# Performance work log

Measured on AMD Instinct MI355X. Metric: run time of the kernel, lower is better.

The kernel has to match this reference:

```python
import jax, jax.numpy as jnp
import numpy as np

D_MODEL = 1024
N_HEADS = 16
N_KV = 4
HEAD_DIM = D_MODEL // N_HEADS  # 64
EPS = 1e-5
THETA = 10000.0


def _rope_tables(S):
    half = HEAD_DIM // 2
    inv_freq = 1.0 / (THETA ** (jnp.arange(half, dtype=jnp.float32) / half))
    t = jnp.arange(S, dtype=jnp.float32)
    f = t[:, None] * inv_freq[None, :]  # [S, half]
    return jnp.cos(f), jnp.sin(f)


def _apply_rope(x, cos, sin):
    # x: [B, H, S, D]
    half = x.shape[-1] // 2
    x1, x2 = x[..., :half], x[..., half:]
    c = cos[None, None, :, :]
    s = sin[None, None, :, :]
    return jnp.concatenate([x1 * c - x2 * s, x1 * s + x2 * c], axis=-1)


def _rmsnorm(x, scale):
    rms = jnp.sqrt(jnp.mean(x * x, axis=-1, keepdims=True) + EPS)
    return x / rms * scale


def setup_inputs() -> dict:
    key = jax.random.key(0)
    ks = jax.random.split(key, 4)
    B, S = 2, 2048
    x = jax.random.normal(ks[0], (B, S, D_MODEL), dtype=jnp.float32)
    Wq = jax.random.normal(ks[1], (D_MODEL, D_MODEL), dtype=jnp.float32) * 0.02
    Wkv = jax.random.normal(ks[2], (D_MODEL, 2 * N_KV * HEAD_DIM), dtype=jnp.float32) * 0.02
    Wo = jax.random.normal(ks[3], (D_MODEL, D_MODEL), dtype=jnp.float32) * 0.02
    q_scale = jnp.ones((HEAD_DIM,), dtype=jnp.float32)
    k_scale = jnp.ones((HEAD_DIM,), dtype=jnp.float32)
    return {"x": x, "Wq": Wq, "Wkv": Wkv, "Wo": Wo,
            "q_scale": q_scale, "k_scale": k_scale}


def reference(x, Wq, Wkv, Wo, q_scale, k_scale):
    B, S, D = x.shape
    groups = N_HEADS // N_KV  # GQA group size

    # projections
    q = (x @ Wq).reshape(B, S, N_HEADS, HEAD_DIM).transpose(0, 2, 1, 3)  # [B,H,S,d]
    kv = x @ Wkv
    k, v = jnp.split(kv, 2, axis=-1)
    k = k.reshape(B, S, N_KV, HEAD_DIM).transpose(0, 2, 1, 3)  # [B,Hkv,S,d]
    v = v.reshape(B, S, N_KV, HEAD_DIM).transpose(0, 2, 1, 3)

    # per-head QK-RMSNorm (before RoPE, as in the torch module)
    q = _rmsnorm(q, q_scale)
    k = _rmsnorm(k, k_scale)

    # RoPE
    cos, sin = _rope_tables(S)
    q = _apply_rope(q, cos, sin)
    k = _apply_rope(k, cos, sin)

    # causal GQA attention (equivalent to SDPA with enable_gqa=True)
    qg = q.reshape(B, N_KV, groups, S, HEAD_DIM)
    scale = 1.0 / np.sqrt(HEAD_DIM).astype(np.float32)
    scores = jnp.einsum('bkgsd,bktd->bkgst', qg, k) * scale  # [B,Hkv,g,S,S]
    causal = jnp.tril(jnp.ones((S, S), dtype=bool))
    scores = jnp.where(causal[None, None, None], scores, -jnp.inf)
    attn = jax.nn.softmax(scores, axis=-1)
    out = jnp.einsum('bkgst,bktd->bkgsd', attn, v)
    out = out.reshape(B, N_HEADS, S, HEAD_DIM).transpose(0, 2, 1, 3).reshape(B, S, D)
    return out @ Wo
```

## Files before the change

kernel.cpp:

```cpp
#include <hip/hip_runtime.h>

#define S_LEN 2048
#define BATCH 2
#define DM    1024
#define NH    16
#define NKV   4
#define HD    64
#define MROWS (BATCH * S_LEN)
#define NQKV  1536

typedef __attribute__((ext_vector_type(8))) short bf16x8;
typedef __attribute__((ext_vector_type(4))) short s16x4;
typedef __attribute__((ext_vector_type(4))) float f32x4;

__device__ __forceinline__ unsigned short f2bf(float f) {
  unsigned int u = __float_as_uint(f);
  u += 0x7FFF + ((u >> 16) & 1);
  return (unsigned short)(u >> 16);
}

__device__ __forceinline__ void gload_lds16(const unsigned short* g, unsigned short* l) {
  __builtin_amdgcn_global_load_lds((const __attribute__((address_space(1))) void*)g,
                                   (__attribute__((address_space(3))) void*)l, 16, 0, 0);
}
__device__ __forceinline__ void gload_lds4(const unsigned short* g, unsigned short* l) {
  __builtin_amdgcn_global_load_lds((const __attribute__((address_space(1))) void*)g,
                                   (__attribute__((address_space(3))) void*)l, 4, 0, 0);
}

__global__ __launch_bounds__(256) void cvt_x_kernel(const float* __restrict__ x,
                                                    unsigned short* __restrict__ xb, int n) {
  int i = (blockIdx.x * 256 + threadIdx.x) * 4;
  if (i < n) {
    float4 v = *reinterpret_cast<const float4*>(x + i);
    xb[i + 0] = f2bf(v.x);
    xb[i + 1] = f2bf(v.y);
    xb[i + 2] = f2bf(v.z);
    xb[i + 3] = f2bf(v.w);
  }
}

__global__ __launch_bounds__(256) void transpose_all_kernel(const float* __restrict__ Wq,
                                                            const float* __restrict__ Wkv,
                                                            const float* __restrict__ Wo,
                                                            unsigned short* __restrict__ wt1,
                                                            unsigned short* __restrict__ wot) {
  __shared__ float tile[64][65];
  int bid = blockIdx.x;
  const float* in;
  unsigned short* out;
  int R, C, bx, by;
  if (bid < 256) { in = Wq; out = wt1; R = 1024; C = 1024; bx = bid & 15; by = bid >> 4; }
  else if (bid < 384) { int k = bid - 256; in = Wkv; out = wt1 + 1024 * 1024; R = 1024; C = 512; bx = k & 7; by = k >> 3; }
  else { int k = bid - 384; in = Wo; out = wot; R = 1024; C = 1024; bx = k & 15; by = k >> 4; }
  int r0 = by * 64, c0 = bx * 64;
  int t = threadIdx.x;
  int rl = t >> 2, cs = (t & 3) * 16;
#pragma unroll
  for (int k = 0; k < 4; ++k) {
    float4 v = *reinterpret_cast<const float4*>(in + (size_t)(r0 + rl) * C + c0 + cs + 4 * k);
    tile[rl][cs + 4 * k + 0] = v.x;
    tile[rl][cs + 4 * k + 1] = v.y;
    tile[rl][cs + 4 * k + 2] = v.z;
    tile[rl][cs + 4 * k + 3] = v.w;
  }
  __syncthreads();
  int cl = t >> 2, rs = (t & 3) * 16;
  bf16x8 v0, v1;
#pragma unroll
  for (int i = 0; i < 8; ++i) v0[i] = (short)f2bf(tile[rs + i][cl]);
#pragma unroll
  for (int i = 0; i < 8; ++i) v1[i] = (short)f2bf(tile[rs + 8 + i][cl]);
  unsigned short* dst = out + (size_t)(c0 + cl) * R + r0 + rs;
  *reinterpret_cast<bf16x8*>(dst) = v0;
  *reinterpret_cast<bf16x8*>(dst + 8) = v1;
}

__global__ __launch_bounds__(256) void gemm1_fused(const unsigned short* __restrict__ A,
                                                   const unsigned short* __restrict__ BT,
                                                   const float* __restrict__ q_scale,
                                                   const float* __restrict__ k_scale,
                                                   unsigned short* __restrict__ qb,
                                                   unsigned short* __restrict__ kbuf,
                                                   unsigned short* __restrict__ vrow,
                                                   int K) {
  __shared__ __align__(16) unsigned short As[128 * 64];
  __shared__ __align__(16) unsigned short Bs[64 * 64];
  int bx = blockIdx.x;
  int row0 = blockIdx.y * 128, col0 = bx * 64;
  int t = threadIdx.x;
  int w = t >> 6, lane = t & 63, quad = lane >> 4, l16 = lane & 15;
  int srow = lane >> 3;
  int scol = (lane & 7) * 8;

  f32x4 acc[2][4];
#pragma unroll
  for (int i = 0; i < 2; ++i)
#pragma unroll
    for (int j = 0; j < 4; ++j) acc[i][j] = (f32x4){0.f, 0.f, 0.f, 0.f};

  for (int k0 = 0; k0 < K; k0 += 64) {
#pragma unroll
    for (int j = 0; j < 4; ++j)
      gload_lds16(A + (size_t)(row0 + w * 32 + j * 8 + srow) * K + k0 + scol,
                  &As[(w * 32 + j * 8) * 64]);
#pragma unroll
    for (int j = 0; j < 2; ++j)
      gload_lds16(BT + (size_t)(col0 + w * 16 + j * 8 + srow) * K + k0 + scol,
                  &Bs[(w * 16 + j * 8) * 64]);
    __syncthreads();
#pragma unroll
    for (int ks = 0; ks < 2; ++ks) {
      bf16x8 af[2], bfr[4];
#pragma unroll
      for (int i = 0; i < 2; ++i)
        af[i] = *reinterpret_cast<const bf16x8*>(&As[(w * 32 + i * 16 + l16) * 64 + ks * 32 + quad * 8]);
#pragma unroll
      for (int j = 0; j < 4; ++j)
        bfr[j] = *reinterpret_cast<const bf16x8*>(&Bs[(j * 16 + l16) * 64 + ks * 32 + quad * 8]);
#pragma unroll
      for (int i = 0; i < 2; ++i)
#pragma unroll
        for (int j = 0; j < 4; ++j)
          acc[i][j] = __builtin_amdgcn_mfma_f32_16x16x32_bf16(af[i], bfr[j], acc[i][j], 0, 0, 0);
    }
    __syncthreads();
  }

  if (bx < 20) {
    const float* scale = (bx < 16) ? q_scale : k_scale;
    float post = (bx < 16) ? 1.0f : 0.125f * 1.44269504088896f;
    float sc0 = scale[l16], sc1 = scale[16 + l16], sc2 = scale[32 + l16], sc3 = scale[48 + l16];
    float invf0 = exp2f((float)l16 * (-13.2877123795495f / 32.0f));
    float invf1 = exp2f((float)(l16 + 16) * (-13.2877123795495f / 32.0f));
#pragma unroll
    for (int i = 0; i < 2; ++i)
#pragma unroll
      for (int rg = 0; rg < 4; ++rg) {
        int row = row0 + w * 32 + i * 16 + quad * 4 + rg;
        int b = row >> 11, s = row & 2047;
        float v0 = acc[i][0][rg], v1 = acc[i][1][rg], v2 = acc[i][2][rg], v3 = acc[i][3][rg];
        float ss = v0 * v0 + v1 * v1 + v2 * v2 + v3 * v3;
        ss += __shfl_xor(ss, 1, 64);
        ss += __shfl_xor(ss, 2, 64);
        ss += __shfl_xor(ss, 4, 64);
        ss += __shfl_xor(ss, 8, 64);
        float inv_rms = 1.0f / sqrtf(ss * (1.0f / 64.0f) + 1e-5f);
        float n0 = v0 * inv_rms * sc0, n1 = v1 * inv_rms * sc1;
        float n2 = v2 * inv_rms * sc2, n3 = v3 * inv_rms * sc3;
        float f0 = (float)s * invf0, f1 = (float)s * invf1;
        float c0 = cosf(f0), s0 = sinf(f0), c1 = cosf(f1), s1 = sinf(f1);
        float o0 = (n0 * c0 - n2 * s0) * post;
        float o1 = (n1 * c1 - n3 * s1) * post;
        float o2 = (n0 * s0 + n2 * c0) * post;
        float o3 = (n1 * s1 + n3 * c1) * post;
        unsigned short* dst = (bx < 16)
            ? qb + ((size_t)(b * NH + bx) * S_LEN + s) * HD
            : kbuf + ((size_t)(b * NKV + (bx - 16)) * S_LEN + s) * HD;
        dst[l16] = f2bf(o0);
        dst[16 + l16] = f2bf(o1);
        dst[32 + l16] = f2bf(o2);
        dst[48 + l16] = f2bf(o3);
      }
  } else {
    int kvh = bx - 20;
#pragma unroll
    for (int i = 0; i < 2; ++i)
#pragma unroll
      for (int rg = 0; rg < 4; ++rg) {
        int row = row0 + w * 32 + i * 16 + quad * 4 + rg;
        unsigned short* dst = vrow + (size_t)row * 256 + kvh * 64;
        dst[l16] = f2bf(acc[i][0][rg]);
        dst[16 + l16] = f2bf(acc[i][1][rg]);
        dst[32 + l16] = f2bf(acc[i][2][rg]);
        dst[48 + l16] = f2bf(acc[i][3][rg]);
      }
  }
}

__global__ __launch_bounds__(256) void v_transpose_bf16(const unsigned short* __restrict__ vrow,
                                                        unsigned short* __restrict__ vt) {
  __shared__ unsigned short tile[64][72];
  int bkv = blockIdx.x >> 5;
  int b = bkv >> 2, kvh = bkv & 3;
  int s0 = (blockIdx.x & 31) * 64;
  int t = threadIdx.x;
  int sl = t >> 2, part = (t & 3) * 16;
  const unsigned short* src = vrow + (size_t)(b * S_LEN + s0 + sl) * 256 + kvh * 64 + part;
  *reinterpret_cast<bf16x8*>(&tile[sl][part]) = *reinterpret_cast<const bf16x8*>(src);
  *reinterpret_cast<bf16x8*>(&tile[sl][part + 8]) = *reinterpret_cast<const bf16x8*>(src + 8);
  __syncthreads();
  int d = t >> 2, sc = (t & 3) * 16;
  bf16x8 a0, a1;
#pragma unroll
  for (int i = 0; i < 8; ++i) a0[i] = (short)tile[sc + i][d];
#pragma unroll
  for (int i = 0; i < 8; ++i) a1[i] = (short)tile[sc + 8 + i][d];
  unsigned short* dst = vt + ((size_t)bkv * 64 + d) * S_LEN + s0 + sc;
  *reinterpret_cast<bf16x8*>(dst) = a0;
  *reinterpret_cast<bf16x8*>(dst + 8) = a1;
}

#define CH 136
#define TILE_SH (32 * CH)
__global__ __launch_bounds__(256, 2) void attn_kernel(const unsigned short* __restrict__ qb,
                                                      const unsigned short* __restrict__ kbuf,
                                                      const unsigned short* __restrict__ vt,
                                                      unsigned short* __restrict__ ctx) {
  __shared__ __align__(16) unsigned short Ks[2][TILE_SH];
  __shared__ __align__(16) unsigned short Vs[2][TILE_SH];
  __shared__ __align__(16) unsigned short PT[4][2][16][72];
  int g = blockIdx.x >> 3;
  int bkv = blockIdx.x & 7;
  int t32 = (g < 32) ? (63 - g) : (g - 32);
  int b = bkv >> 2, kvh = bkv & 3;
  int w = threadIdx.x >> 6;
  int h = kvh * 4 + w;
  int lane = threadIdx.x & 63;
  int quad = lane >> 4, l16 = lane & 15;
  int qa = t32 * 32 + l16;
  const unsigned short* Q = qb + (size_t)(b * NH + h) * S_LEN * HD;
  const unsigned short* Kh = kbuf + (size_t)(b * NKV + kvh) * S_LEN * HD;
  const unsigned short* Vh = vt + (size_t)(b * NKV + kvh) * HD * S_LEN;

  bf16x8 bqa0 = *reinterpret_cast<const bf16x8*>(Q + (size_t)qa * HD + quad * 8);
  bf16x8 bqa1 = *reinterpret_cast<const bf16x8*>(Q + (size_t)qa * HD + 32 + quad * 8);
  bf16x8 bqb0 = *reinterpret_cast<const bf16x8*>(Q + (size_t)(qa + 16) * HD + quad * 8);
  bf16x8 bqb1 = *reinterpret_cast<const bf16x8*>(Q + (size_t)(qa + 16) * HD + 32 + quad * 8);

  bf16x8 ones;
#pragma unroll
  for (int i = 0; i < 8; ++i) ones[i] = (short)0x3F80;

  f32x4 ot[2][4];
#pragma unroll
  for (int gq = 0; gq < 2; ++gq)
#pragma unroll
    for (int i = 0; i < 4; ++i) ot[gq][i] = (f32x4){0.f, 0.f, 0.f, 0.f};
  f32x4 ol[2] = {(f32x4){0.f, 0.f, 0.f, 0.f}, (f32x4){0.f, 0.f, 0.f, 0.f}};

  int nkb = (t32 >> 1) + 1;

  auto stage = [&](int kbase, int dbuf) {
    const unsigned short* kg = Kh + (size_t)(kbase + w * 16) * HD + lane * 2;
    const unsigned short* vg = Vh + (size_t)(w * 16 + (lane >> 5)) * S_LEN + kbase + (lane & 31) * 2;
    unsigned short* kl = &Ks[dbuf][(w * 8) * CH];
    unsigned short* vl = &Vs[dbuf][(w * 8) * CH];
#pragma unroll
    for (int c = 0; c < 8; ++c) {
      gload_lds4(kg + (size_t)(2 * c) * HD, kl + c * CH);
      gload_lds4(vg + (size_t)(2 * c) * S_LEN, vl + c * CH);
    }
  };

  stage(0, 0);
  __syncthreads();

  for (int kbi = 0; kbi < nkb; ++kbi) {
    bool last = (kbi == nkb - 1);
    int kbase = kbi << 6;
    if (!last) stage(kbase + 64, (kbi + 1) & 1);
    const unsigned short* Kd = Ks[kbi & 1];
    const unsigned short* Vd = Vs[kbi & 1];

    f32x4 sa[4], sb[4];
#pragma unroll
    for (int km = 0; km < 4; ++km) {
      int ch = km * 8 + (l16 >> 1);
      int base = ch * CH + (l16 & 1) * 64;
      bf16x8 k0 = *reinterpret_cast<const bf16x8*>(&Kd[base + quad * 8]);
      bf16x8 k1 = *reinterpret_cast<const bf16x8*>(&Kd[base + 32 + quad * 8]);
      f32x4 s = {0.f, 0.f, 0.f, 0.f};
      s = __builtin_amdgcn_mfma_f32_16x16x32_bf16(k0, bqa0, s, 0, 0, 0);
      s = __builtin_amdgcn_mfma_f32_16x16x32_bf16(k1, bqa1, s, 0, 0, 0);
      sa[km] = s;
      f32x4 s2 = {0.f, 0.f, 0.f, 0.f};
      s2 = __builtin_amdgcn_mfma_f32_16x16x32_bf16(k0, bqb0, s2, 0, 0, 0);
      s2 = __builtin_amdgcn_mfma_f32_16x16x32_bf16(k1, bqb1, s2, 0, 0, 0);
      sb[km] = s2;
    }
    if (last) {
#pragma unroll
      for (int km = 0; km < 4; ++km)
#pragma unroll
        for (int rg = 0; rg < 4; ++rg) {
          int key = kbase + km * 16 + quad * 4 + rg;
          if (key > qa) sa[km][rg] = -1e30f;
          if (key > qa + 16) sb[km][rg] = -1e30f;
        }
    }
#pragma unroll
    for (int km = 0; km < 4; ++km) {
      float a0 = exp2f(sa[km][0]), a1 = exp2f(sa[km][1]);
      float a2 = exp2f(sa[km][2]), a3 = exp2f(sa[km][3]);
      uint2 pw;
      pw.x = __builtin_amdgcn_perm(__float_as_uint(a1), __float_as_uint(a0), 0x07060302);
      pw.y = __builtin_amdgcn_perm(__float_as_uint(a3), __float_as_uint(a2), 0x07060302);
      *reinterpret_cast<uint2*>(&PT[w][0][l16][km * 16 + quad * 4]) = pw;
      float b0 = exp2f(sb[km][0]), b1 = exp2f(sb[km][1]);
      float b2 = exp2f(sb[km][2]), b3 = exp2f(sb[km][3]);
      uint2 qw;
      qw.x = __builtin_amdgcn_perm(__float_as_uint(b1), __float_as_uint(b0), 0x07060302);
      qw.y = __builtin_amdgcn_perm(__float_as_uint(b3), __float_as_uint(b2), 0x07060302);
      *reinterpret_cast<uint2*>(&PT[w][1][l16][km * 16 + quad * 4]) = qw;
    }
    bf16x8 pa0 = *reinterpret_cast<const bf16x8*>(&PT[w][0][l16][quad * 8]);
    bf16x8 pa1 = *reinterpret_cast<const bf16x8*>(&PT[w][0][l16][32 + quad * 8]);
    bf16x8 pb0 = *reinterpret_cast<const bf16x8*>(&PT[w][1][l16][quad * 8]);
    bf16x8 pb1 = *reinterpret_cast<const bf16x8*>(&PT[w][1][l16][32 + quad * 8]);
    ol[0] = __builtin_amdgcn_mfma_f32_16x16x32_bf16(ones, pa0, ol[0], 0, 0, 0);
    ol[0] = __builtin_amdgcn_mfma_f32_16x16x32_bf16(ones, pa1, ol[0], 0, 0, 0);
    ol[1] = __builtin_amdgcn_mfma_f32_16x16x32_bf16(ones, pb0, ol[1], 0, 0, 0);
    ol[1] = __builtin_amdgcn_mfma_f32_16x16x32_bf16(ones, pb1, ol[1], 0, 0, 0);
#pragma unroll
    for (int dm = 0; dm < 4; ++dm) {
      int ch = dm * 8 + (l16 >> 1);
      int base = ch * CH + (l16 & 1) * 64;
      bf16x8 v0 = *reinterpret_cast<const bf16x8*>(&Vd[base + quad * 8]);
      bf16x8 v1 = *reinterpret_cast<const bf16x8*>(&Vd[base + 32 + quad * 8]);
      ot[0][dm] = __builtin_amdgcn_mfma_f32_16x16x32_bf16(v0, pa0, ot[0][dm], 0, 0, 0);
      ot[0][dm] = __builtin_amdgcn_mfma_f32_16x16x32_bf16(v1, pa1, ot[0][dm], 0, 0, 0);
      ot[1][dm] = __builtin_amdgcn_mfma_f32_16x16x32_bf16(v0, pb0, ot[1][dm], 0, 0, 0);
      ot[1][dm] = __builtin_amdgcn_mfma_f32_16x16x32_bf16(v1, pb1, ot[1][dm], 0, 0, 0);
    }
    __syncthreads();
  }

#pragma unroll
  for (int gq = 0; gq < 2; ++gq) {
    float inv_l = 1.0f / ol[gq][0];
    size_t base = ((size_t)(b * S_LEN) + qa + gq * 16) * DM + h * HD;
#pragma unroll
    for (int dm = 0; dm < 4; ++dm) {
      s16x4 pv;
#pragma unroll
      for (int rg = 0; rg < 4; ++rg) pv[rg] = (short)f2bf(ot[gq][dm][rg] * inv_l);
      *reinterpret_cast<s16x4*>(ctx + base + dm * 16 + quad * 4) = pv;
    }
  }
}

__global__ __launch_bounds__(256) void gemm_bt_n64(const unsigned short* __restrict__ A,
                                                   const unsigned short* __restrict__ BT,
                                                   float* __restrict__ C,
                                                   int M, int N, int K) {
  __shared__ __align__(16) unsigned short As[128 * 64];
  __shared__ __align__(16) unsigned short Bs[64 * 64];
  int row0 = blockIdx.y * 128, col0 = blockIdx.x * 64;
  int t = threadIdx.x;
  int w = t >> 6, lane = t & 63, quad = lane >> 4, l16 = lane & 15;
  int srow = lane >> 3;
  int scol = (lane & 7) * 8;

  f32x4 acc[2][4];
#pragma unroll
  for (int i = 0; i < 2; ++i)
#pragma unroll
    for (int j = 0; j < 4; ++j) acc[i][j] = (f32x4){0.f, 0.f, 0.f, 0.f};

  for (int k0 = 0; k0 < K; k0 += 64) {
#pragma unroll
    for (int j = 0; j < 4; ++j)
      gload_lds16(A + (size_t)(row0 + w * 32 + j * 8 + srow) * K + k0 + scol,
                  &As[(w * 32 + j * 8) * 64]);
#pragma unroll
    for (int j = 0; j < 2; ++j)
      gload_lds16(BT + (size_t)(col0 + w * 16 + j * 8 + srow) * K + k0 + scol,
                  &Bs[(w * 16 + j * 8) * 64]);
    __syncthreads();
#pragma unroll
    for (int ks = 0; ks < 2; ++ks) {
      bf16x8 af[2], bfr[4];
#pragma unroll
      for (int i = 0; i < 2; ++i)
        af[i] = *reinterpret_cast<const bf16x8*>(&As[(w * 32 + i * 16 + l16) * 64 + ks * 32 + quad * 8]);
#pragma unroll
      for (int j = 0; j < 4; ++j)
        bfr[j] = *reinterpret_cast<const bf16x8*>(&Bs[(j * 16 + l16) * 64 + ks * 32 + quad * 8]);
#pragma unroll
      for (int i = 0; i < 2; ++i)
#pragma unroll
        for (int j = 0; j < 4; ++j)
          acc[i][j] = __builtin_amdgcn_mfma_f32_16x16x32_bf16(af[i], bfr[j], acc[i][j], 0, 0, 0);
    }
    __syncthreads();
  }
#pragma unroll
  for (int i = 0; i < 2; ++i)
#pragma unroll
    for (int j = 0; j < 4; ++j) {
      int row = row0 + w * 32 + i * 16 + quad * 4;
      float* Cptr = C + (size_t)row * N + col0 + j * 16 + l16;
#pragma unroll
      for (int rg = 0; rg < 4; ++rg) Cptr[(size_t)rg * N] = acc[i][j][rg];
    }
}

extern "C" void kernel_launch(void* const* d_in, const int* in_sizes, int n_in,
                              void* d_out, int out_size, void* d_ws, size_t ws_size,
                              hipStream_t stream) {
  const float* x = (const float*)d_in[0];
  const float* Wq = (const float*)d_in[1];
  const float* Wkv = (const float*)d_in[2];
  const float* Wo = (const float*)d_in[3];
  const float* q_scale = (const float*)d_in[4];
  const float* k_scale = (const float*)d_in[5];
  float* out = (float*)d_out;

  char* ws = (char*)d_ws;
  size_t off = 0;
  auto alloc = [&](size_t bytes) {
    void* p = ws + off;
    off += (bytes + 255) & ~(size_t)255;
    return p;
  };
  unsigned short* xb = (unsigned short*)alloc((size_t)MROWS * DM * 2);
  unsigned short* wt1 = (unsigned short*)alloc((size_t)NQKV * DM * 2);
  unsigned short* wot = (unsigned short*)alloc((size_t)DM * DM * 2);
  unsigned short* qb = (unsigned short*)alloc((size_t)BATCH * NH * S_LEN * HD * 2);
  unsigned short* kbuf = (unsigned short*)alloc((size_t)BATCH * NKV * S_LEN * HD * 2);
  unsigned short* vrow = (unsigned short*)alloc((size_t)MROWS * NKV * HD * 2);
  unsigned short* vt = (unsigned short*)alloc((size_t)BATCH * NKV * HD * S_LEN * 2);
  unsigned short* ctx = (unsigned short*)alloc((size_t)MROWS * DM * 2);

  cvt_x_kernel<<<(MROWS * DM) / 1024, 256, 0, stream>>>(x, xb, MROWS * DM);
  transpose_all_kernel<<<640, 256, 0, stream>>>(Wq, Wkv, Wo, wt1, wot);

  gemm1_fused<<<dim3(NQKV / 64, MROWS / 128), 256, 0, stream>>>(xb, wt1, q_scale, k_scale,
                                                                qb, kbuf, vrow, DM);
  v_transpose_bf16<<<256, 256, 0, stream>>>(vrow, vt);

  attn_kernel<<<BATCH * NKV * (S_LEN / 32), 256, 0, stream>>>(qb, kbuf, vt, ctx);

  gemm_bt_n64<<<dim3(DM / 64, MROWS / 128), 256, 0, stream>>>(ctx, wot, out, MROWS, DM, DM);
}
```

Measured before the change: 190.6 us.

## Split attention KV loop across two blocks and combine partials in separate kernel

Measured after the change: 174.9 us. -8.3%, faster.

```diff
diff --git a/kernel.cpp b/kernel.cpp
--- a/kernel.cpp
+++ b/kernel.cpp
@@ -203,16 +203,20 @@
 
 #define CH 136
 #define TILE_SH (32 * CH)
-__global__ __launch_bounds__(256, 2) void attn_kernel(const unsigned short* __restrict__ qb,
+__global__ __launch_bounds__(256, 3) void attn_kernel(const unsigned short* __restrict__ qb,
                                                       const unsigned short* __restrict__ kbuf,
                                                       const unsigned short* __restrict__ vt,
-                                                      unsigned short* __restrict__ ctx) {
+                                                      unsigned short* __restrict__ Opart,
+                                                      float* __restrict__ lpart) {
   __shared__ __align__(16) unsigned short Ks[2][TILE_SH];
   __shared__ __align__(16) unsigned short Vs[2][TILE_SH];
   __shared__ __align__(16) unsigned short PT[4][2][16][72];
-  int g = blockIdx.x >> 3;
-  int bkv = blockIdx.x & 7;
-  int t32 = (g < 32) ? (63 - g) : (g - 32);
+  const size_t OZ = (size_t)BATCH * NH * S_LEN * HD;
+  const size_t LZ = (size_t)BATCH * NH * S_LEN;
+  int t32 = 63 - (int)(blockIdx.x >> 4);
+  int sub = blockIdx.x & 15;
+  int z = sub & 1;
+  int bkv = sub >> 1;
   int b = bkv >> 2, kvh = bkv & 3;
   int w = threadIdx.x >> 6;
   int h = kvh * 4 + w;
@@ -239,7 +243,7 @@
     for (int i = 0; i < 4; ++i) ot[gq][i] = (f32x4){0.f, 0.f, 0.f, 0.f};
   f32x4 ol[2] = {(f32x4){0.f, 0.f, 0.f, 0.f}, (f32x4){0.f, 0.f, 0.f, 0.f}};
 
-  int nkb = (t32 >> 1) + 1;
+  int n = (t32 >> 1) + 1;
 
   auto stage = [&](int kbase, int dbuf) {
     const unsigned short* kg = Kh + (size_t)(kbase + w * 16) * HD + lane * 2;
@@ -253,91 +257,125 @@
     }
   };
 
-  stage(0, 0);
-  __syncthreads();
-
-  for (int kbi = 0; kbi < nkb; ++kbi) {
-    bool last = (kbi == nkb - 1);
-    int kbase = kbi << 6;
-    if (!last) stage(kbase + 64, (kbi + 1) & 1);
-    const unsigned short* Kd = Ks[kbi & 1];
-    const unsigned short* Vd = Vs[kbi & 1];
-
-    f32x4 sa[4], sb[4];
-#pragma unroll
-    for (int km = 0; km < 4; ++km) {
-      int ch = km * 8 + (l16 >> 1);
-      int base = ch * CH + (l16 & 1) * 64;
-      bf16x8 k0 = *reinterpret_cast<const bf16x8*>(&Kd[base + quad * 8]);
-      bf16x8 k1 = *reinterpret_cast<const bf16x8*>(&Kd[base + 32 + quad * 8]);
-      f32x4 s = {0.f, 0.f, 0.f, 0.f};
-      s = __builtin_amdgcn_mfma_f32_16x16x32_bf16(k0, bqa0, s, 0, 0, 0);
-      s = __builtin_amdgcn_mfma_f32_16x16x32_bf16(k1, bqa1, s, 0, 0, 0);
-      sa[km] = s;
-      f32x4 s2 = {0.f, 0.f, 0.f, 0.f};
-      s2 = __builtin_amdgcn_mfma_f32_16x16x32_bf16(k0, bqb0, s2, 0, 0, 0);
-      s2 = __builtin_amdgcn_mfma_f32_16x16x32_bf16(k1, bqb1, s2, 0, 0, 0);
-      sb[km] = s2;
-    }
-    if (last) {
-#pragma unroll
-      for (int km = 0; km < 4; ++km)
-#pragma unroll
-        for (int rg = 0; rg < 4; ++rg) {
-          int key = kbase + km * 16 + quad * 4 + rg;
-          if (key > qa) sa[km][rg] = -1e30f;
-          if (key > qa + 16) sb[km][rg] = -1e30f;
-        }
-    }
-#pragma unroll
-    for (int km = 0; km < 4; ++km) {
-      float a0 = exp2f(sa[km][0]), a1 = exp2f(sa[km][1]);
-      float a2 = exp2f(sa[km][2]), a3 = exp2f(sa[km][3]);
-      uint2 pw;
-      pw.x = __builtin_amdgcn_perm(__float_as_uint(a1), __float_as_uint(a0), 0x07060302);
-      pw.y = __builtin_amdgcn_perm(__float_as_uint(a3), __float_as_uint(a2), 0x07060302);
-      *reinterpret_cast<uint2*>(&PT[w][0][l16][km * 16 + quad * 4]) = pw;
-      float b0 = exp2f(sb[km][0]), b1 = exp2f(sb[km][1]);
-      float b2 = exp2f(sb[km][2]), b3 = exp2f(sb[km][3]);
-      uint2 qw;
-      qw.x = __builtin_amdgcn_perm(__float_as_uint(b1), __float_as_uint(b0), 0x07060302);
-      qw.y = __builtin_amdgcn_perm(__float_as_uint(b3), __float_as_uint(b2), 0x07060302);
-      *reinterpret_cast<uint2*>(&PT[w][1][l16][km * 16 + quad * 4]) = qw;
-    }
-    bf16x8 pa0 = *reinterpret_cast<const bf16x8*>(&PT[w][0][l16][quad * 8]);
-    bf16x8 pa1 = *reinterpret_cast<const bf16x8*>(&PT[w][0][l16][32 + quad * 8]);
-    bf16x8 pb0 = *reinterpret_cast<const bf16x8*>(&PT[w][1][l16][quad * 8]);
-    bf16x8 pb1 = *reinterpret_cast<const bf16x8*>(&PT[w][1][l16][32 + quad * 8]);
-    ol[0] = __builtin_amdgcn_mfma_f32_16x16x32_bf16(ones, pa0, ol[0], 0, 0, 0);
-    ol[0] = __builtin_amdgcn_mfma_f32_16x16x32_bf16(ones, pa1, ol[0], 0, 0, 0);
-    ol[1] = __builtin_amdgcn_mfma_f32_16x16x32_bf16(ones, pb0, ol[1], 0, 0, 0);
-    ol[1] = __builtin_amdgcn_mfma_f32_16x16x32_bf16(ones, pb1, ol[1], 0, 0, 0);
-#pragma unroll
-    for (int dm = 0; dm < 4; ++dm) {
-      int ch = dm * 8 + (l16 >> 1);
-      int base = ch * CH + (l16 & 1) * 64;
-      bf16x8 v0 = *reinterpret_cast<const bf16x8*>(&Vd[base + quad * 8]);
-      bf16x8 v1 = *reinterpret_cast<const bf16x8*>(&Vd[base + 32 + quad * 8]);
-      ot[0][dm] = __builtin_amdgcn_mfma_f32_16x16x32_bf16(v0, pa0, ot[0][dm], 0, 0, 0);
-      ot[0][dm] = __builtin_amdgcn_mfma_f32_16x16x32_bf16(v1, pa1, ot[0][dm], 0, 0, 0);
-      ot[1][dm] = __builtin_amdgcn_mfma_f32_16x16x32_bf16(v0, pb0, ot[1][dm], 0, 0, 0);
-      ot[1][dm] = __builtin_amdgcn_mfma_f32_16x16x32_bf16(v1, pb1, ot[1][dm], 0, 0, 0);
-    }
+  if (z < n) {
+    stage(z << 6, 0);
     __syncthreads();
-  }
-
+
+    for (int kb = z; kb < n; kb += 2) {
+      int dbuf = (kb >> 1) & 1;
+      bool diag = (kb == n - 1);
+      if (kb + 2 < n) stage((kb + 2) << 6, dbuf ^ 1);
+      int kbase = kb << 6;
+      const unsigned short* Kd = Ks[dbuf];
+      const unsigned short* Vd = Vs[dbuf];
+
+      f32x4 sa[4], sb[4];
+#pragma unroll
+      for (int km = 0; km < 4; ++km) {
+        int ch = km * 8 + (l16 >> 1);
+        int base = ch * CH + (l16 & 1) * 64;
+        bf16x8 k0 = *reinterpret_cast<const bf16x8*>(&Kd[base + quad * 8]);
+        bf16x8 k1 = *reinterpret_cast<const bf16x8*>(&Kd[base + 32 + quad * 8]);
+        f32x4 s = {0.f, 0.f, 0.f, 0.f};
+        s = __builtin_amdgcn_mfma_f32_16x16x32_bf16(k0, bqa0, s, 0, 0, 0);
+        s = __builtin_amdgcn_mfma_f32_16x16x32_bf16(k1, bqa1, s, 0, 0, 0);
+        sa[km] = s;
+        f32x4 s2 = {0.f, 0.f, 0.f, 0.f};
+        s2 = __builtin_amdgcn_mfma_f32_16x16x32_bf16(k0, bqb0, s2, 0, 0, 0);
+        s2 = __builtin_amdgcn_mfma_f32_16x16x32_bf16(k1, bqb1, s2, 0, 0, 0);
+        sb[km] = s2;
+      }
+      if (diag) {
+#pragma unroll
+        for (int km = 0; km < 4; ++km)
+#pragma unroll
+          for (int rg = 0; rg < 4; ++rg) {
+            int key = kbase + km * 16 + quad * 4 + rg;
+            if (key > qa) sa[km][rg] = -1e30f;
+            if (key > qa + 16) sb[km][rg] = -1e30f;
+          }
+      }
+#pragma unroll
+      for (int km = 0; km < 4; ++km) {
+        float a0 = exp2f(sa[km][0]), a1 = exp2f(sa[km][1]);
+        float a2 = exp2f(sa[km][2]), a3 = exp2f(sa[km][3]);
+        uint2 pw;
+        pw.x = __builtin_amdgcn_perm(__float_as_uint(a1), __float_as_uint(a0), 0x07060302);
+        pw.y = __builtin_amdgcn_perm(__float_as_uint(a3), __float_as_uint(a2), 0x07060302);
+        *reinterpret_cast<uint2*>(&PT[w][0][l16][km * 16 + quad * 4]) = pw;
+        float b0 = exp2f(sb[km][0]), b1 = exp2f(sb[km][1]);
+        float b2 = exp2f(sb[km][2]), b3 = exp2f(sb[km][3]);
+        uint2 qw;
+        qw.x = __builtin_amdgcn_perm(__float_as_uint(b1), __float_as_uint(b0), 0x07060302);
+        qw.y = __builtin_amdgcn_perm(__float_as_uint(b3), __float_as_uint(b2), 0x07060302);
+        *reinterpret_cast<uint2*>(&PT[w][1][l16][km * 16 + quad * 4]) = qw;
+      }
+      bf16x8 pa0 = *reinterpret_cast<const bf16x8*>(&PT[w][0][l16][quad * 8]);
+      bf16x8 pa1 = *reinterpret_cast<const bf16x8*>(&PT[w][0][l16][32 + quad * 8]);
+      bf16x8 pb0 = *reinterpret_cast<const bf16x8*>(&PT[w][1][l16][quad * 8]);
+      bf16x8 pb1 = *reinterpret_cast<const bf16x8*>(&PT[w][1][l16][32 + quad * 8]);
+      ol[0] = __builtin_amdgcn_mfma_f32_16x16x32_bf16(ones, pa0, ol[0], 0, 0, 0);
+      ol[0] = __builtin_amdgcn_mfma_f32_16x16x32_bf16(ones, pa1, ol[0], 0, 0, 0);
+      ol[1] = __builtin_amdgcn_mfma_f32_16x16x32_bf16(ones, pb0, ol[1], 0, 0, 0);
+      ol[1] = __builtin_amdgcn_mfma_f32_16x16x32_bf16(ones, pb1, ol[1], 0, 0, 0);
+#pragma unroll
+      for (int dm = 0; dm < 4; ++dm) {
+        int ch = dm * 8 + (l16 >> 1);
+        int base = ch * CH + (l16 & 1) * 64;
+        bf16x8 v0 = *reinterpret_cast<const bf16x8*>(&Vd[base + quad * 8]);
+        bf16x8 v1 = *reinterpret_cast<const bf16x8*>(&Vd[base + 32 + quad * 8]);
+        ot[0][dm] = __builtin_amdgcn_mfma_f32_16x16x32_bf16(v0, pa0, ot[0][dm], 0, 0, 0);
+        ot[0][dm] = __builtin_amdgcn_mfma_f32_16x16x32_bf16(v1, pa1, ot[0][dm], 0, 0, 0);
+        ot[1][dm] = __builtin_amdgcn_mfma_f32_16x16x32_bf16(v0, pb0, ot[1][dm], 0, 0, 0);
+        ot[1][dm] = __builtin_amdgcn_mfma_f32_16x16x32_bf16(v1, pb1, ot[1][dm], 0, 0, 0);
+      }
+      __syncthreads();
+    }
+  }
+
+  unsigned short* Oz = Opart + (size_t)z * OZ;
+  float* lz = lpart + (size_t)z * LZ;
 #pragma unroll
   for (int gq = 0; gq < 2; ++gq) {
-    float inv_l = 1.0f / ol[gq][0];
-    size_t base = ((size_t)(b * S_LEN) + qa + gq * 16) * DM + h * HD;
+    size_t base = ((size_t)(b * NH + h) * S_LEN + qa + gq * 16) * HD;
 #pragma unroll
     for (int dm = 0; dm < 4; ++dm) {
       s16x4 pv;
 #pragma unroll
-      for (int rg = 0; rg < 4; ++rg) pv[rg] = (short)f2bf(ot[gq][dm][rg] * inv_l);
-      *reinterpret_cast<s16x4*>(ctx + base + dm * 16 + quad * 4) = pv;
-    }
-  }
+      for (int rg = 0; rg < 4; ++rg) pv[rg] = (short)f2bf(ot[gq][dm][rg]);
+      *reinterpret_cast<s16x4*>(Oz + base + dm * 16 + quad * 4) = pv;
+    }
+  }
+  if (quad == 0) {
+    size_t lb = (size_t)(b * NH + h) * S_LEN + t32 * 32 + l16;
+    lz[lb] = ol[0][0];
+    lz[lb + 16] = ol[1][0];
+  }
+}
+
+__global__ __launch_bounds__(256) void attn_combine_kernel(const unsigned short* __restrict__ Opart,
+                                                           const float* __restrict__ lpart,
+                                                           unsigned short* __restrict__ ctx) {
+  const size_t OZ = (size_t)BATCH * NH * S_LEN * HD;
+  const size_t LZ = (size_t)BATCH * NH * S_LEN;
+  int i8 = blockIdx.x * 256 + threadIdx.x;
+  size_t i = (size_t)i8 * 8;
+  int row = i8 >> 3;
+  bf16x8 a = *reinterpret_cast<const bf16x8*>(Opart + i);
+  bf16x8 c = *reinterpret_cast<const bf16x8*>(Opart + OZ + i);
+  float inv = 1.0f / (lpart[row] + lpart[LZ + row]);
+  int q = row & 2047;
+  int bh = row >> 11;
+  int b = bh >> 4, h = bh & 15;
+  int d0 = (i8 & 7) * 8;
+  bf16x8 o;
+#pragma unroll
+  for (int k = 0; k < 8; ++k) {
+    float fa = __uint_as_float(((unsigned int)(unsigned short)a[k]) << 16);
+    float fc = __uint_as_float(((unsigned int)(unsigned short)c[k]) << 16);
+    o[k] = (short)f2bf((fa + fc) * inv);
+  }
+  *reinterpret_cast<bf16x8*>(ctx + ((size_t)(b * S_LEN + q)) * DM + h * HD + d0) = o;
 }
 
 __global__ __launch_bounds__(256) void gemm_bt_n64(const unsigned short* __restrict__ A,
@@ -422,6 +460,8 @@
   unsigned short* vrow = (unsigned short*)alloc((size_t)MROWS * NKV * HD * 2);
   unsigned short* vt = (unsigned short*)alloc((size_t)BATCH * NKV * HD * S_LEN * 2);
   unsigned short* ctx = (unsigned short*)alloc((size_t)MROWS * DM * 2);
+  unsigned short* Opart = (unsigned short*)alloc(2 * (size_t)BATCH * NH * S_LEN * HD * 2);
+  float* lpart = (float*)alloc(2 * (size_t)BATCH * NH * S_LEN * 4);
 
   cvt_x_kernel<<<(MROWS * DM) / 1024, 256, 0, stream>>>(x, xb, MROWS * DM);
   transpose_all_kernel<<<640, 256, 0, stream>>>(Wq, Wkv, Wo, wt1, wot);
@@ -430,7 +470,8 @@
                                                                 qb, kbuf, vrow, DM);
   v_transpose_bf16<<<256, 256, 0, stream>>>(vrow, vt);
 
-  attn_kernel<<<BATCH * NKV * (S_LEN / 32), 256, 0, stream>>>(qb, kbuf, vt, ctx);
+  attn_kernel<<<1024, 256, 0, stream>>>(qb, kbuf, vt, Opart, lpart);
+  attn_combine_kernel<<<(BATCH * NH * S_LEN * HD / 8) / 256, 256, 0, stream>>>(Opart, lpart, ctx);
 
   gemm_bt_n64<<<dim3(DM / 64, MROWS / 128), 256, 0, stream>>>(ctx, wot, out, MROWS, DM, DM);
 }
```
